# Optimization experiments

Hardware: AMD Instinct MI355X
Metric: run time of the kernel (lower is better)

## Reference

```python
import jax, jax.numpy as jnp
import numpy as np

WH, WW = 8, 8
N = WH * WW
DIM = 128
NUM_HEADS = 4
HEAD_DIM = DIM // NUM_HEADS
SCALE = HEAD_DIM ** -0.5


def _relative_position_index():
    coords = np.stack(np.meshgrid(np.arange(WH), np.arange(WW), indexing='ij'))  # (2, Wh, Ww)
    flat = coords.reshape(2, -1)  # (2, N)
    rel = flat[:, :, None] - flat[:, None, :]  # (2, N, N)
    rel = rel.transpose(1, 2, 0)  # (N, N, 2)
    rel[:, :, 0] += WH - 1
    rel[:, :, 1] += WW - 1
    rel[:, :, 0] *= 2 * WW - 1
    return rel.sum(-1)  # (N, N) int

REL_IDX = _relative_position_index()


def setup_inputs() -> dict:
    key = jax.random.key(0)
    ks = jax.random.split(key, 7)
    B_ = 4096
    nW = 64
    table_size = (2 * WH - 1) * (2 * WW - 1)  # 225
    return {
        'x': jax.random.normal(ks[0], (B_, N, DIM), dtype=jnp.float32),
        'mask': jax.random.normal(ks[1], (nW, N, N), dtype=jnp.float32),
        'qkv_w': jax.random.normal(ks[2], (3 * DIM, DIM), dtype=jnp.float32) * 0.02,
        'qkv_b': jnp.zeros((3 * DIM,), dtype=jnp.float32),
        'proj_w': jax.random.normal(ks[3], (DIM, DIM), dtype=jnp.float32) * 0.02,
        'proj_b': jnp.zeros((DIM,), dtype=jnp.float32),
        'bias_table': jax.random.normal(ks[4], (table_size, NUM_HEADS), dtype=jnp.float32) * 0.02,
    }


def reference(x, mask, qkv_w, qkv_b, proj_w, proj_b, bias_table):
    B_, n, C = x.shape
    nW = mask.shape[0]
    qkv = x @ qkv_w.T + qkv_b  # (B_, N, 3C)
    qkv = qkv.reshape(B_, n, 3, NUM_HEADS, HEAD_DIM)
    q = qkv[:, :, 0] * SCALE  # (B_, N, H, hd)
    k = qkv[:, :, 1]
    v = qkv[:, :, 2]
    attn = jnp.einsum('bihd,bjhd->bhij', q, k)  # (B_, H, N, N)
    rel_bias = bias_table[REL_IDX.reshape(-1)].reshape(n, n, NUM_HEADS)
    attn = attn + rel_bias.transpose(2, 0, 1)[None]  # broadcast over B_
    attn = attn.reshape(B_ // nW, nW, NUM_HEADS, n, n) + mask[None, :, None]
    attn = attn.reshape(B_, NUM_HEADS, n, n)
    attn = jax.nn.softmax(attn, axis=-1)
    out = jnp.einsum('bhij,bjhd->bihd', attn, v).reshape(B_, n, C)
    return out @ proj_w.T + proj_b
```

## Files before the change

kernel.cpp:

```cpp
#include <hip/hip_runtime.h>


typedef __bf16 bf16x8 __attribute__((ext_vector_type(8)));
typedef float f32x16 __attribute__((ext_vector_type(16)));

#define MFMA32(a, b, c) __builtin_amdgcn_mfma_f32_32x32x16_bf16(a, b, c, 0, 0, 0)
#define ATT_SCALE 0.17677669529663687f

__device__ __forceinline__ unsigned short f2bf(float f) {
  union { float fv; unsigned int u; } cv; cv.fv = f;
  unsigned int r = cv.u + 0x7FFFu + ((cv.u >> 16) & 1u);
  return (unsigned short)(r >> 16);
}

__global__ __launch_bounds__(256) void convert_weights(
    const float* __restrict__ qkv_w, const float* __restrict__ proj_w,
    unsigned short* __restrict__ wq, unsigned short* __restrict__ wp) {
  int t = blockIdx.x * 256 + threadIdx.x;
  if (t < 384 * 128) wq[t] = f2bf(qkv_w[t]);
  else               wp[t - 384 * 128] = f2bf(proj_w[t - 384 * 128]);
}

__global__ __launch_bounds__(256) void build_cb(
    const float* __restrict__ mask, const float* __restrict__ bias_table,
    float* __restrict__ cb) {
  int t = blockIdx.x * 256 + threadIdx.x;
  int ij = t & 4095;
  int h = (t >> 12) & 3;
  int w = t >> 14;
  int i = ij >> 6, j = ij & 63;
  int ridx = ((i >> 3) - (j >> 3) + 7) * 15 + ((i & 7) - (j & 7) + 7);
  cb[t] = bias_table[ridx * 4 + h] + mask[(w << 12) + ij];
}

__global__ __launch_bounds__(256, 2) void window_attn(
    const float* __restrict__ x, const float* __restrict__ qkv_b,
    const float* __restrict__ proj_b, const unsigned short* __restrict__ wq,
    const unsigned short* __restrict__ wp, const float* __restrict__ cb,
    float* __restrict__ out, int nW) {
  __shared__ unsigned short Xb[64][136];
  __shared__ unsigned short U[4][7424];

  const int tid = threadIdx.x;
  const int h = tid >> 6;
  const int lane = tid & 63;
  const int l31 = lane & 31;
  const int hl = lane >> 5;
  const int b = blockIdx.x;
  const int w = b % nW;

  const float* xb = x + (size_t)b * 8192;
  #pragma unroll
  for (int it = 0; it < 8; ++it) {
    int e = (it * 256 + tid) * 4;
    float4 v = *reinterpret_cast<const float4*>(xb + e);
    ushort4 o;
    o.x = f2bf(v.x); o.y = f2bf(v.y); o.z = f2bf(v.z); o.w = f2bf(v.w);
    *reinterpret_cast<ushort4*>(&Xb[e >> 7][e & 127]) = o;
  }
  __syncthreads();

  unsigned short* qh = &U[h][0];
  unsigned short* kh = &U[h][2560];
  unsigned short* vh = &U[h][5120];
  unsigned short* ph = &U[h][0];

  #pragma unroll
  for (int s = 0; s < 3; ++s) {
    const int c = s * 128 + h * 32 + l31;
    const float bias = qkv_b[c];
    const unsigned short* wrow = wq + (size_t)c * 128 + hl * 8;
    bf16x8 bfr[8];
    #pragma unroll
    for (int kt = 0; kt < 8; ++kt)
      bfr[kt] = *reinterpret_cast<const bf16x8*>(wrow + kt * 16);
    #pragma unroll
    for (int mt = 0; mt < 2; ++mt) {
      f32x16 acc;
      #pragma unroll
      for (int q = 0; q < 16; ++q) acc[q] = 0.0f;
      #pragma unroll
      for (int kt = 0; kt < 8; ++kt) {
        bf16x8 a = *reinterpret_cast<const bf16x8*>(&Xb[mt * 32 + l31][kt * 16 + hl * 8]);
        acc = MFMA32(a, bfr[kt], acc);
      }
      #pragma unroll
      for (int r = 0; r < 16; ++r) {
        int row = (r & 3) + 8 * (r >> 2) + 4 * hl + mt * 32;
        float val = acc[r] + bias;
        if (s == 0)      qh[row * 40 + l31] = f2bf(val * ATT_SCALE);
        else if (s == 1) kh[row * 40 + l31] = f2bf(val);
        else             vh[l31 * 72 + row] = f2bf(val);
      }
    }
  }
  __syncthreads();

  f32x16 sacc[2][2];
  #pragma unroll
  for (int mt = 0; mt < 2; ++mt)
    #pragma unroll
    for (int jt = 0; jt < 2; ++jt)
      #pragma unroll
      for (int q = 0; q < 16; ++q) sacc[mt][jt][q] = 0.0f;
  #pragma unroll
  for (int kt = 0; kt < 2; ++kt) {
    bf16x8 b0 = *reinterpret_cast<const bf16x8*>(&kh[(l31) * 40 + kt * 16 + hl * 8]);
    bf16x8 b1 = *reinterpret_cast<const bf16x8*>(&kh[(32 + l31) * 40 + kt * 16 + hl * 8]);
    #pragma unroll
    for (int mt = 0; mt < 2; ++mt) {
      bf16x8 a = *reinterpret_cast<const bf16x8*>(&qh[(mt * 32 + l31) * 40 + kt * 16 + hl * 8]);
      sacc[mt][0] = MFMA32(a, b0, sacc[mt][0]);
      sacc[mt][1] = MFMA32(a, b1, sacc[mt][1]);
    }
  }

  const float* cbp = cb + (((size_t)w * 4 + h) << 12);
  float rinv[2][16];
  #pragma unroll
  for (int mt = 0; mt < 2; ++mt) {
    #pragma unroll
    for (int r = 0; r < 16; ++r) {
      int row = (r & 3) + 8 * (r >> 2) + 4 * hl + mt * 32;
      float s0 = sacc[mt][0][r] + cbp[row * 64 + l31];
      float s1 = sacc[mt][1][r] + cbp[row * 64 + 32 + l31];
      float m = fmaxf(s0, s1);
      m = fmaxf(m, __shfl_xor(m, 1));
      m = fmaxf(m, __shfl_xor(m, 2));
      m = fmaxf(m, __shfl_xor(m, 4));
      m = fmaxf(m, __shfl_xor(m, 8));
      m = fmaxf(m, __shfl_xor(m, 16));
      float e0 = __expf(s0 - m);
      float e1 = __expf(s1 - m);
      float sum = e0 + e1;
      sum += __shfl_xor(sum, 1);
      sum += __shfl_xor(sum, 2);
      sum += __shfl_xor(sum, 4);
      sum += __shfl_xor(sum, 8);
      sum += __shfl_xor(sum, 16);
      ph[row * 72 + l31] = f2bf(e0);
      ph[row * 72 + 32 + l31] = f2bf(e1);
      rinv[mt][r] = __builtin_amdgcn_rcpf(sum);
    }
  }

  #pragma unroll
  for (int mt = 0; mt < 2; ++mt) {
    f32x16 oacc;
    #pragma unroll
    for (int q = 0; q < 16; ++q) oacc[q] = 0.0f;
    #pragma unroll
    for (int kt = 0; kt < 4; ++kt) {
      bf16x8 a = *reinterpret_cast<const bf16x8*>(&ph[(mt * 32 + l31) * 72 + kt * 16 + hl * 8]);
      bf16x8 bb = *reinterpret_cast<const bf16x8*>(&vh[l31 * 72 + kt * 16 + hl * 8]);
      oacc = MFMA32(a, bb, oacc);
    }
    #pragma unroll
    for (int r = 0; r < 16; ++r) {
      int row = (r & 3) + 8 * (r >> 2) + 4 * hl + mt * 32;
      Xb[row][h * 32 + l31] = f2bf(oacc[r] * rinv[mt][r]);
    }
  }
  __syncthreads();

  {
    const int c = h * 32 + l31;
    const float pb = proj_b[c];
    const unsigned short* wrow = wp + (size_t)c * 128 + hl * 8;
    bf16x8 bfr[8];
    #pragma unroll
    for (int kt = 0; kt < 8; ++kt)
      bfr[kt] = *reinterpret_cast<const bf16x8*>(wrow + kt * 16);
    float* ob = out + (size_t)b * 8192;
    #pragma unroll
    for (int mt = 0; mt < 2; ++mt) {
      f32x16 acc;
      #pragma unroll
      for (int q = 0; q < 16; ++q) acc[q] = 0.0f;
      #pragma unroll
      for (int kt = 0; kt < 8; ++kt) {
        bf16x8 a = *reinterpret_cast<const bf16x8*>(&Xb[mt * 32 + l31][kt * 16 + hl * 8]);
        acc = MFMA32(a, bfr[kt], acc);
      }
      #pragma unroll
      for (int r = 0; r < 16; ++r) {
        int row = (r & 3) + 8 * (r >> 2) + 4 * hl + mt * 32;
        ob[row * 128 + c] = acc[r] + pb;
      }
    }
  }
}

extern "C" void kernel_launch(void* const* d_in, const int* in_sizes, int n_in,
                              void* d_out, int out_size, void* d_ws, size_t ws_size,
                              hipStream_t stream) {
  const float* x          = (const float*)d_in[0];
  const float* mask       = (const float*)d_in[1];
  const float* qkv_w      = (const float*)d_in[2];
  const float* qkv_b      = (const float*)d_in[3];
  const float* proj_w     = (const float*)d_in[4];
  const float* proj_b     = (const float*)d_in[5];
  const float* bias_table = (const float*)d_in[6];
  const int B_ = in_sizes[0] / 8192;
  const int nW = in_sizes[1] / 4096;

  unsigned short* wq = (unsigned short*)d_ws;
  unsigned short* wp = wq + 384 * 128;
  float* cbuf = (float*)((char*)d_ws + 131072);

  convert_weights<<<(384 * 128 + 128 * 128) / 256, 256, 0, stream>>>(qkv_w, proj_w, wq, wp);
  build_cb<<<(nW * 4 * 4096) / 256, 256, 0, stream>>>(mask, bias_table, cbuf);
  window_attn<<<B_, 256, 0, stream>>>(x, qkv_b, proj_b, wq, wp, cbuf, (float*)d_out, nW);
}
```

Before: 334.8 us.

## Keep Q/K/P in registers via transposed MFMA layouts, cut LDS to raise occupancy

Computes Q, K and V transposed (weights as the A operand), so attention scores come out key-major. The score matrix and the softmax probabilities then go straight from accumulator registers into MFMA fragments through lane shuffles, with no trip through shared memory. Only V^T stays in LDS, which shrinks shared memory and lets launch bounds ask for 4 blocks per CU; the softmax becomes mostly per-lane reductions plus one cross-half shuffle. The attention scale is folded into the Q weights during weight conversion, and the bias/mask buffer is stored transposed to match. The cost is higher register pressure and extra shuffle and packing work, which could cause spills at the new occupancy target.

```diff
diff --git a/kernel.cpp b/kernel.cpp
--- a/kernel.cpp
+++ b/kernel.cpp
@@ -13,12 +13,45 @@
   return (unsigned short)(r >> 16);
 }
 
+__device__ __forceinline__ unsigned pk2(float lo, float hi) {
+  union { __bf16 h[2]; unsigned u; } t;
+  t.h[0] = (__bf16)lo; t.h[1] = (__bf16)hi;
+  return t.u;
+}
+
+__device__ __forceinline__ void pairw(float l0, float l1, float h0, float h1,
+                                      int hl, unsigned &wlo, unsigned &whi) {
+  unsigned lo = pk2(l0, l1);
+  unsigned hi = pk2(h0, h1);
+  unsigned los = (unsigned)__shfl_xor((int)lo, 32);
+  unsigned his = (unsigned)__shfl_xor((int)hi, 32);
+  wlo = hl ? his : lo;
+  whi = hl ? hi : los;
+}
+
+__device__ __forceinline__ bf16x8 frag8(float a0, float a1, float a2, float a3,
+                                        float a4, float a5, float a6, float a7,
+                                        int hl) {
+  union { unsigned u[4]; bf16x8 v; } r;
+  pairw(a0, a1, a4, a5, hl, r.u[0], r.u[2]);
+  pairw(a2, a3, a6, a7, hl, r.u[1], r.u[3]);
+  return r.v;
+}
+
+#define FRAG_LO(p) frag8(p[0], p[1], p[2], p[3], p[4], p[5], p[6], p[7], hl)
+#define FRAG_HI(p) frag8(p[8], p[9], p[10], p[11], p[12], p[13], p[14], p[15], hl)
+
 __global__ __launch_bounds__(256) void convert_weights(
     const float* __restrict__ qkv_w, const float* __restrict__ proj_w,
     unsigned short* __restrict__ wq, unsigned short* __restrict__ wp) {
   int t = blockIdx.x * 256 + threadIdx.x;
-  if (t < 384 * 128) wq[t] = f2bf(qkv_w[t]);
-  else               wp[t - 384 * 128] = f2bf(proj_w[t - 384 * 128]);
+  if (t < 384 * 128) {
+    float v = qkv_w[t];
+    if (t < 128 * 128) v *= ATT_SCALE;
+    wq[t] = f2bf(v);
+  } else {
+    wp[t - 384 * 128] = f2bf(proj_w[t - 384 * 128]);
+  }
 }
 
 __global__ __launch_bounds__(256) void build_cb(
@@ -28,18 +61,18 @@
   int ij = t & 4095;
   int h = (t >> 12) & 3;
   int w = t >> 14;
-  int i = ij >> 6, j = ij & 63;
+  int j = ij >> 6, i = ij & 63;
   int ridx = ((i >> 3) - (j >> 3) + 7) * 15 + ((i & 7) - (j & 7) + 7);
-  cb[t] = bias_table[ridx * 4 + h] + mask[(w << 12) + ij];
-}
-
-__global__ __launch_bounds__(256, 2) void window_attn(
+  cb[t] = bias_table[ridx * 4 + h] + mask[(w << 12) + (i << 6) + j];
+}
+
+__global__ __launch_bounds__(256, 4) void window_attn(
     const float* __restrict__ x, const float* __restrict__ qkv_b,
     const float* __restrict__ proj_b, const unsigned short* __restrict__ wq,
-    const unsigned short* __restrict__ wp, const float* __restrict__ cb,
+    const unsigned short* __restrict__ wp, const float* __restrict__ cbT,
     float* __restrict__ out, int nW) {
   __shared__ unsigned short Xb[64][136];
-  __shared__ unsigned short U[4][7424];
+  __shared__ unsigned short Vt[4][32][72];
 
   const int tid = threadIdx.x;
   const int h = tid >> 6;
@@ -51,115 +84,136 @@
 
   const float* xb = x + (size_t)b * 8192;
   #pragma unroll
-  for (int it = 0; it < 8; ++it) {
-    int e = (it * 256 + tid) * 4;
-    float4 v = *reinterpret_cast<const float4*>(xb + e);
+  for (int st = 0; st < 8; ++st) {
+    int e = (st * 256 + tid) * 4;
+    float4 v4 = *reinterpret_cast<const float4*>(xb + e);
     ushort4 o;
-    o.x = f2bf(v.x); o.y = f2bf(v.y); o.z = f2bf(v.z); o.w = f2bf(v.w);
+    o.x = f2bf(v4.x); o.y = f2bf(v4.y); o.z = f2bf(v4.z); o.w = f2bf(v4.w);
     *reinterpret_cast<ushort4*>(&Xb[e >> 7][e & 127]) = o;
   }
   __syncthreads();
 
-  unsigned short* qh = &U[h][0];
-  unsigned short* kh = &U[h][2560];
-  unsigned short* vh = &U[h][5120];
-  unsigned short* ph = &U[h][0];
-
-  #pragma unroll
-  for (int s = 0; s < 3; ++s) {
-    const int c = s * 128 + h * 32 + l31;
-    const float bias = qkv_b[c];
-    const unsigned short* wrow = wq + (size_t)c * 128 + hl * 8;
-    bf16x8 bfr[8];
-    #pragma unroll
-    for (int kt = 0; kt < 8; ++kt)
-      bfr[kt] = *reinterpret_cast<const bf16x8*>(wrow + kt * 16);
-    #pragma unroll
-    for (int mt = 0; mt < 2; ++mt) {
-      f32x16 acc;
-      #pragma unroll
-      for (int q = 0; q < 16; ++q) acc[q] = 0.0f;
-      #pragma unroll
-      for (int kt = 0; kt < 8; ++kt) {
-        bf16x8 a = *reinterpret_cast<const bf16x8*>(&Xb[mt * 32 + l31][kt * 16 + hl * 8]);
-        acc = MFMA32(a, bfr[kt], acc);
-      }
+  {
+    f32x16 av0, av1;
+    #pragma unroll
+    for (int q = 0; q < 16; ++q) { av0[q] = 0.0f; av1[q] = 0.0f; }
+    const unsigned short* wvp = wq + (size_t)(256 + h * 32 + l31) * 128 + hl * 8;
+    #pragma unroll
+    for (int kt = 0; kt < 8; ++kt) {
+      bf16x8 aw = *reinterpret_cast<const bf16x8*>(wvp + kt * 16);
+      bf16x8 b0 = *reinterpret_cast<const bf16x8*>(&Xb[l31][kt * 16 + hl * 8]);
+      bf16x8 b1 = *reinterpret_cast<const bf16x8*>(&Xb[32 + l31][kt * 16 + hl * 8]);
+      av0 = MFMA32(aw, b0, av0);
+      av1 = MFMA32(aw, b1, av1);
+    }
+    #pragma unroll
+    for (int r = 0; r < 16; ++r) {
+      int dr = (r & 3) + 8 * (r >> 2) + 4 * hl;
+      float bv = qkv_b[256 + h * 32 + dr];
+      Vt[h][dr][l31]      = f2bf(av0[r] + bv);
+      Vt[h][dr][32 + l31] = f2bf(av1[r] + bv);
+    }
+  }
+
+  f32x16 aq[2], ak[2];
+  #pragma unroll
+  for (int t2 = 0; t2 < 2; ++t2)
+    #pragma unroll
+    for (int q = 0; q < 16; ++q) { aq[t2][q] = 0.0f; ak[t2][q] = 0.0f; }
+  {
+    const unsigned short* wqp = wq + (size_t)(h * 32 + l31) * 128 + hl * 8;
+    const unsigned short* wkp = wq + (size_t)(128 + h * 32 + l31) * 128 + hl * 8;
+    #pragma unroll
+    for (int kt = 0; kt < 8; ++kt) {
+      bf16x8 b0 = *reinterpret_cast<const bf16x8*>(&Xb[l31][kt * 16 + hl * 8]);
+      bf16x8 b1 = *reinterpret_cast<const bf16x8*>(&Xb[32 + l31][kt * 16 + hl * 8]);
+      bf16x8 awq = *reinterpret_cast<const bf16x8*>(wqp + kt * 16);
+      bf16x8 awk = *reinterpret_cast<const bf16x8*>(wkp + kt * 16);
+      aq[0] = MFMA32(awq, b0, aq[0]);
+      aq[1] = MFMA32(awq, b1, aq[1]);
+      ak[0] = MFMA32(awk, b0, ak[0]);
+      ak[1] = MFMA32(awk, b1, ak[1]);
+    }
+  }
+  __syncthreads();
+
+  #pragma unroll
+  for (int r = 0; r < 16; ++r) {
+    int dr = (r & 3) + 8 * (r >> 2) + 4 * hl;
+    float bq = qkv_b[h * 32 + dr] * ATT_SCALE;
+    float bk = qkv_b[128 + h * 32 + dr];
+    aq[0][r] += bq; aq[1][r] += bq;
+    ak[0][r] += bk; ak[1][r] += bk;
+  }
+
+  bf16x8 qf[2][2], kf[2][2];
+  #pragma unroll
+  for (int t2 = 0; t2 < 2; ++t2) {
+    qf[t2][0] = FRAG_LO(aq[t2]); qf[t2][1] = FRAG_HI(aq[t2]);
+    kf[t2][0] = FRAG_LO(ak[t2]); kf[t2][1] = FRAG_HI(ak[t2]);
+  }
+
+  f32x16 sacc[2][2];
+  #pragma unroll
+  for (int mt = 0; mt < 2; ++mt)
+    #pragma unroll
+    for (int it = 0; it < 2; ++it) {
+      #pragma unroll
+      for (int q = 0; q < 16; ++q) sacc[mt][it][q] = 0.0f;
+      sacc[mt][it] = MFMA32(kf[mt][0], qf[it][0], sacc[mt][it]);
+      sacc[mt][it] = MFMA32(kf[mt][1], qf[it][1], sacc[mt][it]);
+    }
+
+  const float* cbp = cbT + (((size_t)w * 4 + h) << 12);
+  float rinv[2];
+  #pragma unroll
+  for (int it = 0; it < 2; ++it) {
+    #pragma unroll
+    for (int mt = 0; mt < 2; ++mt)
       #pragma unroll
       for (int r = 0; r < 16; ++r) {
-        int row = (r & 3) + 8 * (r >> 2) + 4 * hl + mt * 32;
-        float val = acc[r] + bias;
-        if (s == 0)      qh[row * 40 + l31] = f2bf(val * ATT_SCALE);
-        else if (s == 1) kh[row * 40 + l31] = f2bf(val);
-        else             vh[l31 * 72 + row] = f2bf(val);
-      }
-    }
-  }
-  __syncthreads();
-
-  f32x16 sacc[2][2];
-  #pragma unroll
-  for (int mt = 0; mt < 2; ++mt)
-    #pragma unroll
-    for (int jt = 0; jt < 2; ++jt)
-      #pragma unroll
-      for (int q = 0; q < 16; ++q) sacc[mt][jt][q] = 0.0f;
-  #pragma unroll
-  for (int kt = 0; kt < 2; ++kt) {
-    bf16x8 b0 = *reinterpret_cast<const bf16x8*>(&kh[(l31) * 40 + kt * 16 + hl * 8]);
-    bf16x8 b1 = *reinterpret_cast<const bf16x8*>(&kh[(32 + l31) * 40 + kt * 16 + hl * 8]);
-    #pragma unroll
-    for (int mt = 0; mt < 2; ++mt) {
-      bf16x8 a = *reinterpret_cast<const bf16x8*>(&qh[(mt * 32 + l31) * 40 + kt * 16 + hl * 8]);
-      sacc[mt][0] = MFMA32(a, b0, sacc[mt][0]);
-      sacc[mt][1] = MFMA32(a, b1, sacc[mt][1]);
-    }
-  }
-
-  const float* cbp = cb + (((size_t)w * 4 + h) << 12);
-  float rinv[2][16];
-  #pragma unroll
-  for (int mt = 0; mt < 2; ++mt) {
-    #pragma unroll
-    for (int r = 0; r < 16; ++r) {
-      int row = (r & 3) + 8 * (r >> 2) + 4 * hl + mt * 32;
-      float s0 = sacc[mt][0][r] + cbp[row * 64 + l31];
-      float s1 = sacc[mt][1][r] + cbp[row * 64 + 32 + l31];
-      float m = fmaxf(s0, s1);
-      m = fmaxf(m, __shfl_xor(m, 1));
-      m = fmaxf(m, __shfl_xor(m, 2));
-      m = fmaxf(m, __shfl_xor(m, 4));
-      m = fmaxf(m, __shfl_xor(m, 8));
-      m = fmaxf(m, __shfl_xor(m, 16));
-      float e0 = __expf(s0 - m);
-      float e1 = __expf(s1 - m);
-      float sum = e0 + e1;
-      sum += __shfl_xor(sum, 1);
-      sum += __shfl_xor(sum, 2);
-      sum += __shfl_xor(sum, 4);
-      sum += __shfl_xor(sum, 8);
-      sum += __shfl_xor(sum, 16);
-      ph[row * 72 + l31] = f2bf(e0);
-      ph[row * 72 + 32 + l31] = f2bf(e1);
-      rinv[mt][r] = __builtin_amdgcn_rcpf(sum);
-    }
-  }
-
-  #pragma unroll
-  for (int mt = 0; mt < 2; ++mt) {
-    f32x16 oacc;
-    #pragma unroll
-    for (int q = 0; q < 16; ++q) oacc[q] = 0.0f;
-    #pragma unroll
-    for (int kt = 0; kt < 4; ++kt) {
-      bf16x8 a = *reinterpret_cast<const bf16x8*>(&ph[(mt * 32 + l31) * 72 + kt * 16 + hl * 8]);
-      bf16x8 bb = *reinterpret_cast<const bf16x8*>(&vh[l31 * 72 + kt * 16 + hl * 8]);
-      oacc = MFMA32(a, bb, oacc);
-    }
-    #pragma unroll
-    for (int r = 0; r < 16; ++r) {
-      int row = (r & 3) + 8 * (r >> 2) + 4 * hl + mt * 32;
-      Xb[row][h * 32 + l31] = f2bf(oacc[r] * rinv[mt][r]);
-    }
+        int jr = (r & 3) + 8 * (r >> 2) + 4 * hl + 32 * mt;
+        sacc[mt][it][r] += cbp[jr * 64 + 32 * it + l31];
+      }
+    float m = sacc[0][it][0];
+    #pragma unroll
+    for (int mt = 0; mt < 2; ++mt)
+      #pragma unroll
+      for (int r = 0; r < 16; ++r) m = fmaxf(m, sacc[mt][it][r]);
+    m = fmaxf(m, __shfl_xor(m, 32));
+    float sum = 0.0f;
+    #pragma unroll
+    for (int mt = 0; mt < 2; ++mt)
+      #pragma unroll
+      for (int r = 0; r < 16; ++r) {
+        float e = __expf(sacc[mt][it][r] - m);
+        sacc[mt][it][r] = e;
+        sum += e;
+      }
+    sum += __shfl_xor(sum, 32);
+    rinv[it] = __builtin_amdgcn_rcpf(sum);
+  }
+
+  bf16x8 pf0[4], pf1[4];
+  pf0[0] = FRAG_LO(sacc[0][0]); pf0[1] = FRAG_HI(sacc[0][0]);
+  pf0[2] = FRAG_LO(sacc[1][0]); pf0[3] = FRAG_HI(sacc[1][0]);
+  pf1[0] = FRAG_LO(sacc[0][1]); pf1[1] = FRAG_HI(sacc[0][1]);
+  pf1[2] = FRAG_LO(sacc[1][1]); pf1[3] = FRAG_HI(sacc[1][1]);
+
+  f32x16 o0, o1;
+  #pragma unroll
+  for (int q = 0; q < 16; ++q) { o0[q] = 0.0f; o1[q] = 0.0f; }
+  #pragma unroll
+  for (int kt = 0; kt < 4; ++kt) {
+    bf16x8 aV = *reinterpret_cast<const bf16x8*>(&Vt[h][l31][kt * 16 + hl * 8]);
+    o0 = MFMA32(aV, pf0[kt], o0);
+    o1 = MFMA32(aV, pf1[kt], o1);
+  }
+  #pragma unroll
+  for (int r = 0; r < 16; ++r) {
+    int dr = (r & 3) + 8 * (r >> 2) + 4 * hl;
+    Xb[l31][h * 32 + dr]      = f2bf(o0[r] * rinv[0]);
+    Xb[32 + l31][h * 32 + dr] = f2bf(o1[r] * rinv[1]);
   }
   __syncthreads();
 
```

New measurement: 366.4 us. 9.4% more time.
